# Kernel optimization log

Hardware: AMD Instinct MI355X
Metric: run time of the kernel (lower is better)

## Reference

```python
import jax, jax.numpy as jnp
import numpy as np

D_IN = 2048
D_OUT = 2048
D_HIDDEN = 16384
K = 64
N_TOKENS = 8192


def setup_inputs() -> dict:
    key = jax.random.key(0)
    ks = jax.random.split(key, 8)
    # kaiming-uniform-ish scale: bound = sqrt(6 / fan_in) (gain for a=sqrt(5) omitted; scale only)
    def kaiming(k, shape):
        fan_in = shape[1]
        bound = float(np.sqrt(1.0 / fan_in))
        return jax.random.uniform(k, shape, jnp.float32, -bound, bound)
    return {
        "mlp_input": jax.random.normal(ks[0], (N_TOKENS, D_IN), jnp.float32),
        "mlp_output_target": jax.random.normal(ks[1], (N_TOKENS, D_OUT), jnp.float32),
        "W_enc": kaiming(ks[2], (D_HIDDEN, D_IN)),
        "b_enc": jnp.zeros((D_HIDDEN,), jnp.float32),
        "W_dec": kaiming(ks[3], (D_OUT, D_HIDDEN)),
        "b_dec": jnp.zeros((D_OUT,), jnp.float32),
        "W_skip": jnp.eye(D_OUT, D_IN, dtype=jnp.float32),  # nn.init.eye_ when d_in == d_out
        "b_skip": jnp.zeros((D_OUT,), jnp.float32),
        "k": K,
    }


def reference(mlp_input, mlp_output_target, W_enc, b_enc, W_dec, b_dec, W_skip, b_skip, k):
    # encode: pre-activations [N, d_hidden]
    pre_acts = mlp_input @ W_enc.T + b_enc
    # topk activation: keep top-k per token, relu them, scatter into zeros
    topk_vals, topk_idx = jax.lax.top_k(pre_acts, k)
    topk_vals = jax.nn.relu(topk_vals)
    rows = jnp.arange(pre_acts.shape[0])[:, None]  # [N,1] broadcast against [N,k]
    h = jnp.zeros_like(pre_acts).at[rows, topk_idx].set(topk_vals)
    # decode + skip connection
    mlp_output_hat = h @ W_dec.T + b_dec + mlp_input @ W_skip.T + b_skip
    loss = jnp.mean(jnp.square(mlp_output_hat - mlp_output_target))
    return mlp_output_hat, h, loss
```

## Files before the change

kernel.cpp:

```cpp
#include <hip/hip_runtime.h>
#include <stdint.h>

#define NT   8192
#define DI   2048
#define DH   16384
#define DO   2048
#define KSEL 64
#define EPS_SEL 0.004f
#define BCAP 256

typedef _Float16 f16;
typedef f16  f16x8 __attribute__((ext_vector_type(8)));
typedef float f32x4 __attribute__((ext_vector_type(4)));
typedef unsigned short usx8 __attribute__((ext_vector_type(8)));

__device__ __forceinline__ unsigned short f2h_bits(float x){
  f16 h = (f16)x;
  union { f16 h; unsigned short u; } c; c.h = h; return c.u;
}
__device__ __forceinline__ float h_bits2f(unsigned short u){
  union { unsigned short u; f16 h; } c; c.u = u; return (float)c.h;
}
__device__ __forceinline__ unsigned char f2fp8(float x){
  return (unsigned char)(__builtin_amdgcn_cvt_pk_fp8_f32(x, 0.f, 0u, false) & 0xff);
}

__device__ __forceinline__ void gload16(const void* g, void* lds){
  __builtin_amdgcn_global_load_lds(
    (const __attribute__((address_space(1))) void*)(uintptr_t)g,
    (__attribute__((address_space(3))) void*)(uint32_t)(uintptr_t)lds,
    16, 0, 0);
}

__global__ __launch_bounds__(256) void k_cvt(const float* __restrict__ in,
                                             unsigned short* __restrict__ out, int n8)
{
  int i = blockIdx.x*256 + threadIdx.x;
  if (i >= n8) return;
  const float4* p = (const float4*)in + (size_t)i*2;
  float4 a = p[0], b = p[1];
  union { f16 h[8]; usx8 u; } r;
  r.h[0]=(f16)a.x; r.h[1]=(f16)a.y; r.h[2]=(f16)a.z; r.h[3]=(f16)a.w;
  r.h[4]=(f16)b.x; r.h[5]=(f16)b.y; r.h[6]=(f16)b.z; r.h[7]=(f16)b.w;
  ((usx8*)out)[i] = r.u;
}

__global__ __launch_bounds__(256) void k_transpose_cvt8(const float* __restrict__ W,
                                                        unsigned char* __restrict__ WT)
{
  __shared__ unsigned char t[64][68];
  const int r0 = blockIdx.x*64;
  const int c0 = blockIdx.y*64;
  const int tid = threadIdx.x;
  const int q = tid >> 6, s = tid & 63;
#pragma unroll
  for (int i=0;i<16;i++){
    int r = q + i*4;
    t[r][s] = f2fp8(W[(size_t)(r0+r)*DH + c0 + s] * 64.0f);
  }
  __syncthreads();
#pragma unroll
  for (int i=0;i<16;i++){
    int c = q + i*4;
    WT[(size_t)(c0+c)*DO + r0 + s] = t[s][c];
  }
}

template<bool F16OUT, bool HASB2>
__device__ __forceinline__ void gemm8_body(
    const unsigned short* __restrict__ Ap,
    const unsigned short* __restrict__ Bp,
    const float* __restrict__ bias1,
    const float* __restrict__ bias2,
    void* __restrict__ Cout, int N)
{
  __shared__ unsigned short lds[65536];
  const int tid  = threadIdx.x;
  const int lane = tid & 63;
  const int wv   = tid >> 6;
  const int wm   = wv >> 2;
  const int wn   = wv & 3;
  const int bm   = blockIdx.x;
  const int bn   = blockIdx.y;
  const int fr   = lane & 15;
  const int fq   = lane >> 4;

  f32x4 acc[8][4];
#pragma unroll
  for (int i=0;i<8;i++)
#pragma unroll
    for (int j=0;j<4;j++) acc[i][j] = (f32x4){0.f,0.f,0.f,0.f};

  f16x8 ar[4][2];
  f16x8 br[2][2];

#define STAGE_HALF(t, ab, h) do { \
    const unsigned short* G_ = (ab) ? Bp : Ap; \
    const int rb_ = ((ab) ? bn : bm)*256 + (h)*128; \
    const int k0_ = (t)*64; \
    const int db_ = ((t)&1)*32768 + (ab)*16384 + (h)*8192; \
    _Pragma("unroll") \
    for (int is_=0; is_<2; ++is_){ \
      const int cw_ = wv*64 + is_*512; \
      const int cl_ = cw_ + lane; \
      const int cs_ = cl_ ^ ((cl_>>3)&7); \
      gload16(G_ + (size_t)(rb_ + (cs_>>3))*DI + k0_ + (cs_&7)*8, \
              (unsigned short*)lds + db_ + cw_*8); \
    } } while(0)

#define LD_A(buf, mh) do { \
    const int ba_ = (buf)*32768 + (mh)*8192; \
    _Pragma("unroll") \
    for (int mf_=0; mf_<4; ++mf_) \
    _Pragma("unroll") \
    for (int ks_=0; ks_<2; ++ks_){ \
      const int lin_ = (wm*64 + mf_*16 + fr)*128 + (ks_*4 + fq)*16; \
      const int sz_  = lin_ ^ ((((lin_>>7)&7))<<4); \
      ar[mf_][ks_] = *(const f16x8*)&lds[ba_ + (sz_>>1)]; \
    } } while(0)

#define LD_B(buf, nh) do { \
    const int bb_ = (buf)*32768 + 16384 + (nh)*8192; \
    _Pragma("unroll") \
    for (int nf_=0; nf_<2; ++nf_) \
    _Pragma("unroll") \
    for (int ks_=0; ks_<2; ++ks_){ \
      const int lin_ = (wn*32 + nf_*16 + fr)*128 + (ks_*4 + fq)*16; \
      const int sz_  = lin_ ^ ((((lin_>>7)&7))<<4); \
      br[nf_][ks_] = *(const f16x8*)&lds[bb_ + (sz_>>1)]; \
    } } while(0)

#define MM(mh, nh) do { \
    _Pragma("unroll") \
    for (int mf_=0; mf_<4; ++mf_) \
    _Pragma("unroll") \
    for (int nf_=0; nf_<2; ++nf_) \
    _Pragma("unroll") \
    for (int ks_=0; ks_<2; ++ks_) \
      acc[(mh)*4+mf_][(nh)*2+nf_] = __builtin_amdgcn_mfma_f32_16x16x32_f16( \
          ar[mf_][ks_], br[nf_][ks_], acc[(mh)*4+mf_][(nh)*2+nf_], 0, 0, 0); \
  } while(0)

#define VM6 asm volatile("s_waitcnt vmcnt(6)" ::: "memory")
#define VM0 asm volatile("s_waitcnt vmcnt(0)" ::: "memory")

#define PH(buf, mh, nh, LA_, LB_, STG, VM) do { \
    if (LA_) LD_A(buf, mh); \
    if (LB_) LD_B(buf, nh); \
    STG; \
    VM; \
    __builtin_amdgcn_s_barrier(); \
    asm volatile("s_waitcnt lgkmcnt(0)" ::: "memory"); \
    __builtin_amdgcn_sched_barrier(0); \
    __builtin_amdgcn_s_setprio(1); \
    MM(mh, nh); \
    __builtin_amdgcn_s_setprio(0); \
  } while(0)

  STAGE_HALF(0,0,0); STAGE_HALF(0,1,1); STAGE_HALF(0,0,1); STAGE_HALF(0,1,0);
  STAGE_HALF(1,0,0); STAGE_HALF(1,1,1); STAGE_HALF(1,0,1);
  asm volatile("s_waitcnt vmcnt(6)" ::: "memory");
  __builtin_amdgcn_s_barrier();

  for (int j = 0; j < 15; ++j) {
    const int a = 2*j, b = 2*j+1;
    PH(0, 0,0, 1,1, STAGE_HALF(b,  1,0), (void)0);
    PH(0, 0,1, 0,1, STAGE_HALF(a+2,0,0), (void)0);
    PH(0, 1,1, 1,0, STAGE_HALF(a+2,1,1), (void)0);
    PH(0, 1,0, 0,1, STAGE_HALF(a+2,0,1), VM6);
    PH(1, 0,0, 1,1, STAGE_HALF(a+2,1,0), (void)0);
    PH(1, 0,1, 0,1, STAGE_HALF(b+2,0,0), (void)0);
    PH(1, 1,1, 1,0, STAGE_HALF(b+2,1,1), (void)0);
    PH(1, 1,0, 0,1, STAGE_HALF(b+2,0,1), VM6);
  }
  PH(0, 0,0, 1,1, STAGE_HALF(31,1,0), (void)0);
  PH(0, 0,1, 0,1, (void)0, (void)0);
  PH(0, 1,1, 1,0, (void)0, (void)0);
  PH(0, 1,0, 0,1, (void)0, VM0);
  PH(1, 0,0, 1,1, (void)0, (void)0);
  PH(1, 0,1, 0,1, (void)0, (void)0);
  PH(1, 1,1, 1,0, (void)0, (void)0);
  PH(1, 1,0, 0,1, (void)0, (void)0);

#undef PH
#undef VM6
#undef VM0
#undef MM
#undef LD_B
#undef LD_A
#undef STAGE_HALF

#pragma unroll
  for (int nh=0; nh<2; ++nh)
#pragma unroll
  for (int nf=0; nf<2; ++nf){
    const int col = bn*256 + nh*128 + wn*32 + nf*16 + fr;
    float bs = bias1[col];
    if (HASB2) bs += bias2[col];
#pragma unroll
    for (int mh=0; mh<2; ++mh)
#pragma unroll
    for (int mf=0; mf<4; ++mf){
      const int row0 = bm*256 + mh*128 + wm*64 + mf*16 + fq*4;
#pragma unroll
      for (int q=0; q<4; ++q){
        float v = acc[mh*4+mf][nh*2+nf][q] + bs;
        if (F16OUT) ((unsigned short*)Cout)[(size_t)(row0+q)*N + col] = f2h_bits(v);
        else        ((float*)Cout)[(size_t)(row0+q)*N + col] = v;
      }
    }
  }
}

__global__ __launch_bounds__(512, 2) void k_gemm_enc8(
    const unsigned short* __restrict__ Ap, const unsigned short* __restrict__ Bp,
    const float* __restrict__ bias, unsigned short* __restrict__ C)
{
  gemm8_body<true, false>(Ap, Bp, bias, nullptr, (void*)C, DH);
}

__global__ __launch_bounds__(512, 2) void k_gemm_skip8(
    const unsigned short* __restrict__ Ap, const unsigned short* __restrict__ Bp,
    const float* __restrict__ bias1, const float* __restrict__ bias2,
    float* __restrict__ C)
{
  gemm8_body<false, true>(Ap, Bp, bias1, bias2, (void*)C, DO);
}

__global__ __launch_bounds__(256) void k_topk(
    const unsigned short* __restrict__ P,
    const float* __restrict__ X,
    const float* __restrict__ Wenc,
    const float* __restrict__ benc,
    int*   __restrict__ candIdx,
    float* __restrict__ candVal)
{
  __shared__ unsigned int hist8[8][257];
  __shared__ unsigned int hist2[257];
  __shared__ int   inIdx[64];
  __shared__ float inVal[64];
  __shared__ int    bandIdx[BCAP];
  __shared__ double bandVal[BCAP];
  __shared__ int s_inCnt, s_bandCnt, s_sel, s_above, s_sel2;

  const int r = blockIdx.x;
  const int tid = threadIdx.x;
  const int wv = tid >> 6, lane = tid & 63;
  const int lc = lane & 7;
  const unsigned short* Prow = P + (size_t)r*DH;

#pragma unroll
  for (int k=0;k<8;k++) hist8[k][tid] = 0;
  hist2[tid] = 0;
  if (tid==0){ s_inCnt=0; s_bandCnt=0; }

  const usx8* Pv = (const usx8*)Prow;
  usx8 c0 = Pv[tid];        usx8 c1 = Pv[tid+256];
  usx8 c2 = Pv[tid+512];    usx8 c3 = Pv[tid+768];
  usx8 c4 = Pv[tid+1024];   usx8 c5 = Pv[tid+1280];
  usx8 c6 = Pv[tid+1536];   usx8 c7 = Pv[tid+1792];
  __syncthreads();

#define OMAP(b) (unsigned short)(((b) & 0x8000) ? (unsigned short)~(b) : (unsigned short)((b)|0x8000))
#define H1(CC) { _Pragma("unroll") for (int e=0;e<8;e++){ \
    unsigned short o = OMAP(CC[e]); atomicAdd(&hist8[lc][o>>8], 1u); } }
  H1(c0) H1(c1) H1(c2) H1(c3) H1(c4) H1(c5) H1(c6) H1(c7)
#undef H1
  __syncthreads();
  {
    unsigned int hs = 0;
#pragma unroll
    for (int c=0;c<8;c++) hs += hist8[c][tid];
    hist8[0][tid] = hs;
  }
  __syncthreads();

  if (tid < 64) {
    const int h0 = 255 - 4*tid;
    unsigned int c0_=hist8[0][h0], c1_=hist8[0][h0-1], c2_=hist8[0][h0-2], c3_=hist8[0][h0-3];
    unsigned int s = c0_+c1_+c2_+c3_;
    unsigned int Pi = s;
#pragma unroll
    for (int off=1; off<64; off<<=1){
      unsigned int t = __shfl_up(Pi, off);
      if (tid >= off) Pi += t;
    }
    unsigned long long mk = __ballot(Pi >= KSEL);
    int cr = (int)__builtin_ctzll(mk);
    if (tid == cr){
      unsigned int cum = Pi - s;
      unsigned int cc[4] = {c0_,c1_,c2_,c3_};
#pragma unroll
      for (int j=0;j<4;j++){
        if (cum + cc[j] >= KSEL){ s_sel = h0-j; s_above = (int)cum; break; }
        cum += cc[j];
      }
    }
  }
  __syncthreads();
  const int bsel = s_sel; const int cntAbove = s_above;

#define H2(CC) { _Pragma("unroll") for (int e=0;e<8;e++){ \
    unsigned short o = OMAP(CC[e]); \
    if ((int)(o>>8) == bsel) atomicAdd(&hist2[o & 0xff], 1u); } }
  H2(c0) H2(c1) H2(c2) H2(c3) H2(c4) H2(c5) H2(c6) H2(c7)
#undef H2
  __syncthreads();
  {
    const int K2 = KSEL - cntAbove;
    if (tid < 64) {
      const int h0 = 255 - 4*tid;
      unsigned int c0_=hist2[h0], c1_=hist2[h0-1], c2_=hist2[h0-2], c3_=hist2[h0-3];
      unsigned int s = c0_+c1_+c2_+c3_;
      unsigned int Pi = s;
#pragma unroll
      for (int off=1; off<64; off<<=1){
        unsigned int t = __shfl_up(Pi, off);
        if (tid >= off) Pi += t;
      }
      unsigned long long mk = __ballot(Pi >= (unsigned)K2);
      int cr = (int)__builtin_ctzll(mk);
      if (tid == cr){
        unsigned int cum = Pi - s;
        unsigned int cc[4] = {c0_,c1_,c2_,c3_};
#pragma unroll
        for (int j=0;j<4;j++){
          if (cum + cc[j] >= (unsigned)K2){ s_sel2 = h0-j; break; }
          cum += cc[j];
        }
      }
    }
  }
  __syncthreads();

  unsigned short To = (unsigned short)((bsel<<8) | s_sel2);
  unsigned short tb = (To & 0x8000) ? (unsigned short)(To ^ 0x8000) : (unsigned short)~To;
  const float T = h_bits2f(tb);
  const float hiv = T + 2.0f*EPS_SEL, lov = T - 2.0f*EPS_SEL;

#define EXT(CC, KK) { _Pragma("unroll") for (int e=0;e<8;e++){ \
    float v = h_bits2f(CC[e]); \
    if (v > hiv){ \
      int p = atomicAdd(&s_inCnt,1); \
      if (p < 64){ inIdx[p] = (tid + (KK)*256)*8 + e; inVal[p] = v; } \
    } else if (v >= lov){ \
      int p = atomicAdd(&s_bandCnt,1); \
      if (p < BCAP) bandIdx[p] = (tid + (KK)*256)*8 + e; \
    } } }
  EXT(c0,0) EXT(c1,1) EXT(c2,2) EXT(c3,3) EXT(c4,4) EXT(c5,5) EXT(c6,6) EXT(c7,7)
#undef EXT
#undef OMAP
  __syncthreads();
  const int m = s_inCnt < 64 ? s_inCnt : 64;
  const int B = s_bandCnt < BCAP ? s_bandCnt : BCAP;

  const float* Xr = X + (size_t)r*DI;
  for (int b=wv; b<B; b+=4){
    const int j = bandIdx[b];
    const float* Wr = Wenc + (size_t)j*DI;
    double s0=0.0, s1=0.0, s2=0.0, s3=0.0;
    for (int k0=lane; k0<DI; k0+=256){
      s0 = fma((double)Xr[k0],     (double)Wr[k0],     s0);
      s1 = fma((double)Xr[k0+64],  (double)Wr[k0+64],  s1);
      s2 = fma((double)Xr[k0+128], (double)Wr[k0+128], s2);
      s3 = fma((double)Xr[k0+192], (double)Wr[k0+192], s3);
    }
    double s = (s0+s1)+(s2+s3);
#pragma unroll
    for (int off=32; off>=1; off>>=1) s += __shfl_down(s, off);
    if (lane==0) bandVal[b] = s + (double)benc[j];
  }
  __syncthreads();

  int* ci = candIdx + (size_t)r*KSEL;
  float* cv = candVal + (size_t)r*KSEL;
  for (int t=tid; t<m; t+=256){ ci[t]=inIdx[t]; cv[t]=inVal[t]; }

  const int need = KSEL - m;
  if (tid < 64 && need > 0){
    unsigned int used = 0;
    for (int t=0;t<need;t++){
      double best = -1.0e300; int bi = -1;
#pragma unroll
      for (int sIt=0;sIt<4;sIt++){
        int b = tid + sIt*64;
        if (b < B && !((used>>sIt)&1)){
          double v = bandVal[b];
          if (v > best){ best=v; bi=b; }
        }
      }
#pragma unroll
      for (int off=32; off>=1; off>>=1){
        double ov = __shfl_down(best, off);
        int    oi = __shfl_down(bi,   off);
        if (ov > best){ best = ov; bi = oi; }
      }
      bi   = __shfl(bi, 0);
      best = __shfl(best, 0);
      if ((bi & 63) == tid) used |= 1u << (bi >> 6);
      if (tid == 0){
        ci[m+t] = bandIdx[bi];
        cv[m+t] = (float)best;
      }
    }
  }
}

__global__ __launch_bounds__(256) void k_decode(
    float* __restrict__ outhat,
    const unsigned char* __restrict__ WdT8,
    const int*   __restrict__ candIdx,
    const float* __restrict__ candVal,
    const float* __restrict__ target,
    float* __restrict__ lossPartial)
{
  __shared__ int   sIdx[KSEL];
  __shared__ float sVal[KSEL];
  __shared__ float wsum[4];
  const int r = blockIdx.x, tid = threadIdx.x;
  if (tid < KSEL){
    sIdx[tid]=candIdx[(size_t)r*KSEL+tid];
    float v=candVal[(size_t)r*KSEL+tid];
    sVal[tid] = (v>0.f ? v : 0.f) * 0.015625f;
  }
  __syncthreads();
  float* orow = outhat + (size_t)r*DO;
  float a[8];
  {
    float4 v0 = *(const float4*)(orow + tid*8);
    float4 v1 = *(const float4*)(orow + tid*8 + 4);
    a[0]=v0.x;a[1]=v0.y;a[2]=v0.z;a[3]=v0.w;a[4]=v1.x;a[5]=v1.y;a[6]=v1.z;a[7]=v1.w;
  }
#pragma unroll 4
  for (int c=0;c<KSEL;c++){
    const float v = sVal[c];
    const uint2 w = *(const uint2*)(WdT8 + (size_t)sIdx[c]*DO + tid*8);
    a[0] = fmaf(v, __builtin_amdgcn_cvt_f32_fp8(w.x, 0), a[0]);
    a[1] = fmaf(v, __builtin_amdgcn_cvt_f32_fp8(w.x, 1), a[1]);
    a[2] = fmaf(v, __builtin_amdgcn_cvt_f32_fp8(w.x, 2), a[2]);
    a[3] = fmaf(v, __builtin_amdgcn_cvt_f32_fp8(w.x, 3), a[3]);
    a[4] = fmaf(v, __builtin_amdgcn_cvt_f32_fp8(w.y, 0), a[4]);
    a[5] = fmaf(v, __builtin_amdgcn_cvt_f32_fp8(w.y, 1), a[5]);
    a[6] = fmaf(v, __builtin_amdgcn_cvt_f32_fp8(w.y, 2), a[6]);
    a[7] = fmaf(v, __builtin_amdgcn_cvt_f32_fp8(w.y, 3), a[7]);
  }
  const float* trow = target + (size_t)r*DO;
  float4 t0 = *(const float4*)(trow + tid*8);
  float4 t1 = *(const float4*)(trow + tid*8 + 4);
  float tt[8] = {t0.x,t0.y,t0.z,t0.w,t1.x,t1.y,t1.z,t1.w};
  float ls = 0.f;
#pragma unroll
  for (int j=0;j<8;j++){ float d = a[j]-tt[j]; ls = fmaf(d,d,ls); }
  {
    float4 v0 = {a[0],a[1],a[2],a[3]}, v1 = {a[4],a[5],a[6],a[7]};
    *(float4*)(orow + tid*8) = v0;
    *(float4*)(orow + tid*8 + 4) = v1;
  }
#pragma unroll
  for (int off=32; off>=1; off>>=1) ls += __shfl_down(ls, off);
  if ((tid&63)==0) wsum[tid>>6]=ls;
  __syncthreads();
  if (tid==0)
    lossPartial[r] = (wsum[0]+wsum[1]+wsum[2]+wsum[3]) * (1.0f/((float)NT*(float)DO));
}

__global__ __launch_bounds__(256) void k_lossreduce(const float* __restrict__ lp,
                                                    float* __restrict__ out)
{
  __shared__ double ws[4];
  double s=0.0;
  for (int i=threadIdx.x;i<NT;i+=256) s += (double)lp[i];
#pragma unroll
  for (int off=32; off>=1; off>>=1) s += __shfl_down(s, off);
  if ((threadIdx.x&63)==0) ws[threadIdx.x>>6]=s;
  __syncthreads();
  if (threadIdx.x==0) *out = (float)(ws[0]+ws[1]+ws[2]+ws[3]);
}

__global__ __launch_bounds__(256) void k_scatter(
    float* __restrict__ H, const int* __restrict__ candIdx, const float* __restrict__ candVal)
{
  const int r=blockIdx.x, tid=threadIdx.x;
  float* hr = H + (size_t)r*DH;
  const float4 z = {0.f,0.f,0.f,0.f};
#pragma unroll
  for (int i=0;i<16;i++) ((float4*)hr)[tid + i*256] = z;
  __syncthreads();
  if (tid<KSEL){
    float v = candVal[(size_t)r*KSEL+tid];
    hr[candIdx[(size_t)r*KSEL+tid]] = v>0.f ? v : 0.f;
  }
}

extern "C" void kernel_launch(void* const* d_in, const int* in_sizes, int n_in,
                              void* d_out, int out_size, void* d_ws, size_t ws_size,
                              hipStream_t stream)
{
  const float* X     = (const float*)d_in[0];
  const float* tgt   = (const float*)d_in[1];
  const float* Wenc  = (const float*)d_in[2];
  const float* benc  = (const float*)d_in[3];
  const float* Wdec  = (const float*)d_in[4];
  const float* bdec  = (const float*)d_in[5];
  const float* Wskip = (const float*)d_in[6];
  const float* bskip = (const float*)d_in[7];

  float* out     = (float*)d_out;
  float* outhat  = out;
  float* H       = out + (size_t)NT*DO;
  float* lossOut = out + (size_t)NT*DO + (size_t)NT*DH;

  char* hb = (char*)H;
  unsigned short* P      = (unsigned short*)hb;
  char* U                = hb + (size_t)NT*DH*2;
  unsigned short* Xh     = (unsigned short*)U;
  unsigned short* Wench  = (unsigned short*)(U + (size_t)NT*DI*2);
  unsigned short* Wskiph = (unsigned short*)(U + (size_t)NT*DI*2 + (size_t)DH*DI*2);
  unsigned char*  WdT8   = (unsigned char*)(U + (size_t)NT*DI*2 + (size_t)DH*DI*2 + (size_t)DO*DI*2);

  int*   candIdx    = (int*)d_ws;
  float* candVal    = (float*)((char*)d_ws + (size_t)NT*KSEL*4);
  float* lossPartial= (float*)((char*)d_ws + (size_t)NT*KSEL*8);

  k_cvt<<<NT*DI/8/256, 256, 0, stream>>>(X, Xh, NT*DI/8);
  k_cvt<<<DH*DI/8/256, 256, 0, stream>>>(Wenc, Wench, DH*DI/8);
  k_cvt<<<DO*DI/8/256, 256, 0, stream>>>(Wskip, Wskiph, DO*DI/8);
  k_transpose_cvt8<<<dim3(DO/64, DH/64), 256, 0, stream>>>(Wdec, WdT8);

  k_gemm_enc8<<<dim3(NT/256, DH/256), 512, 0, stream>>>(Xh, Wench, benc, P);
  k_topk<<<NT, 256, 0, stream>>>(P, X, Wenc, benc, candIdx, candVal);
  k_gemm_skip8<<<dim3(NT/256, DO/256), 512, 0, stream>>>(Xh, Wskiph, bdec, bskip, outhat);
  k_decode<<<NT, 256, 0, stream>>>(outhat, WdT8, candIdx, candVal, tgt, lossPartial);
  k_lossreduce<<<1, 256, 0, stream>>>(lossPartial, lossOut);
  k_scatter<<<NT, 256, 0, stream>>>(H, candIdx, candVal);
}
```

Baseline: 1.152 ms.

## Double-buffer LDS fragment registers to overlap next-phase loads with MFMA

Splits the A/B register fragments into even/odd sets so the LDS reads for the next phase are issued before the current phase's MFMAs, and waits with a partial lgkmcnt instead of draining all LDS loads. This hides LDS read latency behind matrix math in the GEMM main loop. It costs extra VGPRs, which may lower occupancy or cause spills, and the hand-tuned lgkmcnt counts must match the issued loads exactly or results will be wrong.

```diff
diff --git a/kernel.cpp b/kernel.cpp
--- a/kernel.cpp
+++ b/kernel.cpp
@@ -91,8 +91,8 @@
 #pragma unroll
     for (int j=0;j<4;j++) acc[i][j] = (f32x4){0.f,0.f,0.f,0.f};
 
-  f16x8 ar[4][2];
-  f16x8 br[2][2];
+  f16x8 arE[4][2], arO[4][2];
+  f16x8 brE[2][2], brO[2][2];
 
 #define STAGE_HALF(t, ab, h) do { \
     const unsigned short* G_ = (ab) ? Bp : Ap; \
@@ -108,7 +108,7 @@
               (unsigned short*)lds + db_ + cw_*8); \
     } } while(0)
 
-#define LD_A(buf, mh) do { \
+#define LD_A(S, buf, mh) do { \
     const int ba_ = (buf)*32768 + (mh)*8192; \
     _Pragma("unroll") \
     for (int mf_=0; mf_<4; ++mf_) \
@@ -116,10 +116,10 @@
     for (int ks_=0; ks_<2; ++ks_){ \
       const int lin_ = (wm*64 + mf_*16 + fr)*128 + (ks_*4 + fq)*16; \
       const int sz_  = lin_ ^ ((((lin_>>7)&7))<<4); \
-      ar[mf_][ks_] = *(const f16x8*)&lds[ba_ + (sz_>>1)]; \
+      ar##S[mf_][ks_] = *(const f16x8*)&lds[ba_ + (sz_>>1)]; \
     } } while(0)
 
-#define LD_B(buf, nh) do { \
+#define LD_B(S, buf, nh) do { \
     const int bb_ = (buf)*32768 + 16384 + (nh)*8192; \
     _Pragma("unroll") \
     for (int nf_=0; nf_<2; ++nf_) \
@@ -127,10 +127,10 @@
     for (int ks_=0; ks_<2; ++ks_){ \
       const int lin_ = (wn*32 + nf_*16 + fr)*128 + (ks_*4 + fq)*16; \
       const int sz_  = lin_ ^ ((((lin_>>7)&7))<<4); \
-      br[nf_][ks_] = *(const f16x8*)&lds[bb_ + (sz_>>1)]; \
+      br##S[nf_][ks_] = *(const f16x8*)&lds[bb_ + (sz_>>1)]; \
     } } while(0)
 
-#define MM(mh, nh) do { \
+#define MM(AS, BS, mh, nh) do { \
     _Pragma("unroll") \
     for (int mf_=0; mf_<4; ++mf_) \
     _Pragma("unroll") \
@@ -138,51 +138,54 @@
     _Pragma("unroll") \
     for (int ks_=0; ks_<2; ++ks_) \
       acc[(mh)*4+mf_][(nh)*2+nf_] = __builtin_amdgcn_mfma_f32_16x16x32_f16( \
-          ar[mf_][ks_], br[nf_][ks_], acc[(mh)*4+mf_][(nh)*2+nf_], 0, 0, 0); \
+          ar##AS[mf_][ks_], br##BS[nf_][ks_], acc[(mh)*4+mf_][(nh)*2+nf_], 0, 0, 0); \
   } while(0)
 
 #define VM6 asm volatile("s_waitcnt vmcnt(6)" ::: "memory")
 #define VM0 asm volatile("s_waitcnt vmcnt(0)" ::: "memory")
 
-#define PH(buf, mh, nh, LA_, LB_, STG, VM) do { \
-    if (LA_) LD_A(buf, mh); \
-    if (LB_) LD_B(buf, nh); \
-    STG; \
+#define PHX(AS, BS, mh, nh, PRE, STG, VM, LGN) do { \
     VM; \
     __builtin_amdgcn_s_barrier(); \
-    asm volatile("s_waitcnt lgkmcnt(0)" ::: "memory"); \
+    PRE; \
+    STG; \
+    asm volatile("s_waitcnt lgkmcnt(" #LGN ")" ::: "memory"); \
     __builtin_amdgcn_sched_barrier(0); \
     __builtin_amdgcn_s_setprio(1); \
-    MM(mh, nh); \
+    MM(AS, BS, mh, nh); \
     __builtin_amdgcn_s_setprio(0); \
   } while(0)
+
+#define NOP2 do {} while(0)
 
   STAGE_HALF(0,0,0); STAGE_HALF(0,1,1); STAGE_HALF(0,0,1); STAGE_HALF(0,1,0);
   STAGE_HALF(1,0,0); STAGE_HALF(1,1,1); STAGE_HALF(1,0,1);
   asm volatile("s_waitcnt vmcnt(6)" ::: "memory");
   __builtin_amdgcn_s_barrier();
+  LD_A(E, 0, 0); LD_B(E, 0, 0);
 
   for (int j = 0; j < 15; ++j) {
     const int a = 2*j, b = 2*j+1;
-    PH(0, 0,0, 1,1, STAGE_HALF(b,  1,0), (void)0);
-    PH(0, 0,1, 0,1, STAGE_HALF(a+2,0,0), (void)0);
-    PH(0, 1,1, 1,0, STAGE_HALF(a+2,1,1), (void)0);
-    PH(0, 1,0, 0,1, STAGE_HALF(a+2,0,1), VM6);
-    PH(1, 0,0, 1,1, STAGE_HALF(a+2,1,0), (void)0);
-    PH(1, 0,1, 0,1, STAGE_HALF(b+2,0,0), (void)0);
-    PH(1, 1,1, 1,0, STAGE_HALF(b+2,1,1), (void)0);
-    PH(1, 1,0, 0,1, STAGE_HALF(b+2,0,1), VM6);
-  }
-  PH(0, 0,0, 1,1, STAGE_HALF(31,1,0), (void)0);
-  PH(0, 0,1, 0,1, (void)0, (void)0);
-  PH(0, 1,1, 1,0, (void)0, (void)0);
-  PH(0, 1,0, 0,1, (void)0, VM0);
-  PH(1, 0,0, 1,1, (void)0, (void)0);
-  PH(1, 0,1, 0,1, (void)0, (void)0);
-  PH(1, 1,1, 1,0, (void)0, (void)0);
-  PH(1, 1,0, 0,1, (void)0, (void)0);
-
-#undef PH
+    PHX(E,E, 0,0, LD_B(O,0,1),                STAGE_HALF(b,  1,0), NOP2, 4);
+    PHX(E,O, 0,1, LD_A(O,0,1),                STAGE_HALF(a+2,0,0), NOP2, 8);
+    PHX(O,O, 1,1, LD_B(E,0,0),                STAGE_HALF(a+2,1,1), NOP2, 4);
+    PHX(O,E, 1,0, LD_A(E,1,0); LD_B(O,1,0),   STAGE_HALF(a+2,0,1), VM6, 12);
+    PHX(E,O, 0,0, LD_B(E,1,1),                STAGE_HALF(a+2,1,0), NOP2, 4);
+    PHX(E,E, 0,1, LD_A(O,1,1),                STAGE_HALF(b+2,0,0), NOP2, 8);
+    PHX(O,E, 1,1, LD_B(O,1,0),                STAGE_HALF(b+2,1,1), NOP2, 4);
+    PHX(O,O, 1,0, LD_A(E,0,0); LD_B(E,0,0),   STAGE_HALF(b+2,0,1), VM6, 12);
+  }
+  PHX(E,E, 0,0, LD_B(O,0,1),                STAGE_HALF(31,1,0), NOP2, 4);
+  PHX(E,O, 0,1, LD_A(O,0,1),                NOP2,               NOP2, 8);
+  PHX(O,O, 1,1, LD_B(E,0,0),                NOP2,               NOP2, 4);
+  PHX(O,E, 1,0, LD_A(E,1,0); LD_B(O,1,0),   NOP2,               VM0, 12);
+  PHX(E,O, 0,0, LD_B(E,1,1),                NOP2,               NOP2, 4);
+  PHX(E,E, 0,1, LD_A(O,1,1),                NOP2,               NOP2, 8);
+  PHX(O,E, 1,1, LD_B(O,1,0),                NOP2,               NOP2, 4);
+  PHX(O,O, 1,0, NOP2,                       NOP2,               NOP2, 0);
+
+#undef NOP2
+#undef PHX
 #undef VM6
 #undef VM0
 #undef MM
```

Result: slower. 2.130 ms (+85.0%).
